# Kernel tuning notes

Hardware: AMD Instinct MI355X
Metric: run time of the kernel (lower is better)

## Reference

```python
import jax, jax.numpy as jnp
import numpy as np
import math

B, S, D, H = 1, 2048, 2048, 16
HD = D // H  # head_dim = 128


def _rotate_half(x):
    h = x.shape[-1] // 2
    return jnp.concatenate([-x[..., h:], x[..., :h]], axis=-1)


def setup_inputs() -> dict:
    key = jax.random.key(0)
    ks = jax.random.split(key, 8)
    hidden_states = jax.random.normal(ks[0], (B, S, D), dtype=jnp.float32)
    # additive causal mask: 0 on/below diagonal, large negative above
    causal = jnp.tril(jnp.ones((S, S), dtype=bool))
    attention_mask = jnp.where(causal, 0.0, -1e9).astype(jnp.float32)[None, None]
    # LLaMA rotary tables for head_dim
    inv_freq = 1.0 / (10000.0 ** (jnp.arange(0, HD, 2, dtype=jnp.float32) / HD))
    t = jnp.arange(S, dtype=jnp.float32)
    freqs = jnp.einsum('s,d->sd', t, inv_freq)          # [S, HD/2]
    emb = jnp.concatenate([freqs, freqs], axis=-1)       # [S, HD]
    cos = jnp.cos(emb)[None, None]                       # [1,1,S,HD]
    sin = jnp.sin(emb)[None, None]
    scale = 1.0 / math.sqrt(D)
    Wq = jax.random.normal(ks[1], (D, D), dtype=jnp.float32) * scale
    Wk = jax.random.normal(ks[2], (D, D), dtype=jnp.float32) * scale
    Wv = jax.random.normal(ks[3], (D, D), dtype=jnp.float32) * scale
    Wo = jax.random.normal(ks[4], (D, D), dtype=jnp.float32) * scale
    # IA3 scales initialized to ones (as in module), perturbed slightly to be non-trivial
    l_k = jnp.ones((1, H, 1, HD), dtype=jnp.float32) + 0.01 * jax.random.normal(ks[5], (1, H, 1, HD), dtype=jnp.float32)
    l_v = jnp.ones((1, H, 1, HD), dtype=jnp.float32) + 0.01 * jax.random.normal(ks[6], (1, H, 1, HD), dtype=jnp.float32)
    return {
        'hidden_states': hidden_states, 'attention_mask': attention_mask,
        'cos': cos, 'sin': sin,
        'Wq': Wq, 'Wk': Wk, 'Wv': Wv, 'Wo': Wo, 'l_k': l_k, 'l_v': l_v,
    }


def reference(hidden_states, attention_mask, cos, sin, Wq, Wk, Wv, Wo, l_k, l_v):
    b, s, d = hidden_states.shape
    h, hd = H, HD
    # projections (nn.Linear: x @ W.T), split heads -> [b, h, s, hd]
    def split_heads(x):
        return x.reshape(b, s, h, hd).transpose(0, 2, 1, 3)
    q = split_heads(hidden_states @ Wq.T)
    k = split_heads(hidden_states @ Wk.T)
    v = split_heads(hidden_states @ Wv.T)
    # RoPE on q and k
    q = q * cos + _rotate_half(q) * sin
    k = k * cos + _rotate_half(k) * sin
    # IA3: note the module scales QUERY by peft_l_k and VALUE by peft_l_v
    q = q * l_k
    v = v * l_v
    # manual attention
    scores = jnp.einsum('bhqd,bhkd->bhqk', q, k) / math.sqrt(hd)
    scores = scores + attention_mask
    attn = jax.nn.softmax(scores.astype(jnp.float32), axis=-1).astype(scores.dtype)
    out = jnp.einsum('bhqk,bhkd->bhqd', attn, v)
    out = out.transpose(0, 2, 1, 3).reshape(b, s, d)
    return out @ Wo.T
```

## Files before the change

kernel.cpp:

```cpp
#include <hip/hip_runtime.h>

typedef __attribute__((ext_vector_type(8))) short short8;
typedef __attribute__((ext_vector_type(4))) short s16x4;
typedef __attribute__((ext_vector_type(4))) float f32x4;
typedef unsigned short ushort;

#define S_LEN 2048
#define D_MODEL 2048
#define NH 16
#define HD 128

__device__ __forceinline__ float b2f(ushort u) {
  union { unsigned int i; float f; } v; v.i = ((unsigned int)u) << 16; return v.f;
}
__device__ __forceinline__ ushort f2b(float f) {
  union { float f; unsigned int i; } v; v.f = f;
  unsigned int r = v.i + 0x7FFFu + ((v.i >> 16) & 1u);
  return (ushort)(r >> 16);
}
__device__ __forceinline__ ushort f2b_trunc(float f) {
  union { float f; unsigned int i; } v; v.f = f;
  return (ushort)(v.i >> 16);
}

__device__ __forceinline__ void gload_lds16(const void* g, void* l) {
  __builtin_amdgcn_global_load_lds(
      (const __attribute__((address_space(1))) void*)g,
      (__attribute__((address_space(3))) void*)l, 16, 0, 0);
}

template<bool C32, bool QKV>
__device__ __forceinline__ void gemm_bf16_body(const ushort* __restrict__ A,
                                               const ushort* __restrict__ B,
                                               void* __restrict__ Cp, int ldc,
                                               const float* __restrict__ lv)
{
  __shared__ ushort lA[128 * 64];
  __shared__ ushort lB[128 * 64];
  const int tid  = threadIdx.x;
  const int lane = tid & 63;
  const int wave = tid >> 6;
  const int quad = lane >> 4;
  const int l15  = lane & 15;
  const int wm   = wave >> 1;
  const int wn   = wave & 1;
  const int m0   = blockIdx.y * 128;
  const int n0   = blockIdx.x * 128;

  f32x4 acc[4][4];
#pragma unroll
  for (int i = 0; i < 4; ++i)
#pragma unroll
    for (int j = 0; j < 4; ++j)
      acc[i][j] = (f32x4){0.f, 0.f, 0.f, 0.f};

  const int srow0 = wave * 8 + (lane >> 3);
  const int cph   = lane & 7;

  for (int kt = 0; kt < 32; ++kt) {
    __syncthreads();
#pragma unroll
    for (int j = 0; j < 4; ++j) {
      const int row = j * 32 + srow0;
      const int gc  = cph ^ (row & 7);
      gload_lds16(A + (size_t)(m0 + row) * 2048 + kt * 64 + gc * 8,
                  &lA[row * 64 + cph * 8]);
      gload_lds16(B + (size_t)(n0 + row) * 2048 + kt * 64 + gc * 8,
                  &lB[row * 64 + cph * 8]);
    }
    __syncthreads();
#pragma unroll
    for (int kk = 0; kk < 2; ++kk) {
      short8 af[4], bfr[4];
#pragma unroll
      for (int i = 0; i < 4; ++i) {
        const int r = wm * 64 + i * 16 + l15;
        af[i] = *(const short8*)&lA[r * 64 + (((kk * 4 + quad) ^ (l15 & 7)) * 8)];
      }
#pragma unroll
      for (int j = 0; j < 4; ++j) {
        const int r = wn * 64 + j * 16 + l15;
        bfr[j] = *(const short8*)&lB[r * 64 + (((kk * 4 + quad) ^ (l15 & 7)) * 8)];
      }
#pragma unroll
      for (int i = 0; i < 4; ++i)
#pragma unroll
        for (int j = 0; j < 4; ++j)
          acc[i][j] = __builtin_amdgcn_mfma_f32_16x16x32_bf16(af[i], bfr[j], acc[i][j], 0, 0, 0);
    }
  }

  if (QKV && n0 >= 4096) {
    ushort* C = (ushort*)Cp;
#pragma unroll
    for (int j = 0; j < 4; ++j)
#pragma unroll
      for (int i = 0; i < 4; ++i) {
        const int vcol = n0 - 4096 + wn * 64 + j * 16 + l15;
        const float sc = lv[vcol];
        const int sb   = m0 + wm * 64 + i * 16 + quad * 4;
        s16x4 pk;
#pragma unroll
        for (int r = 0; r < 4; ++r) pk[r] = (short)f2b(acc[i][j][r] * sc);
        *(s16x4*)&C[(size_t)vcol * 6144 + 4096 + sb] = pk;
      }
    return;
  }

#pragma unroll
  for (int i = 0; i < 4; ++i)
#pragma unroll
    for (int j = 0; j < 4; ++j)
#pragma unroll
      for (int r = 0; r < 4; ++r) {
        const int row = m0 + wm * 64 + i * 16 + quad * 4 + r;
        const int col = n0 + wn * 64 + j * 16 + l15;
        if (C32) ((float*)Cp)[(size_t)row * ldc + col] = acc[i][j][r];
        else     ((ushort*)Cp)[(size_t)row * ldc + col] = f2b(acc[i][j][r]);
      }
}

__global__ __launch_bounds__(256)
void gemm_qkv_b(const ushort* __restrict__ A, const ushort* __restrict__ B,
                ushort* __restrict__ C, const float* __restrict__ lv)
{ gemm_bf16_body<false, true>(A, B, C, 6144, lv); }

__global__ __launch_bounds__(256)
void gemm_bf16_f(const ushort* __restrict__ A, const ushort* __restrict__ B,
                 float* __restrict__ C, int ldc)
{ gemm_bf16_body<true, false>(A, B, C, ldc, nullptr); }

__global__ __launch_bounds__(256)
void cvt_to_bf16(const float* __restrict__ hs, const float* __restrict__ Wq,
                 const float* __restrict__ Wk, const float* __restrict__ Wv,
                 const float* __restrict__ Wo, ushort* __restrict__ dst)
{
  const size_t base = ((size_t)blockIdx.x * 256 + threadIdx.x) * 8;
  const int row = (int)(base >> 11);
  const int col = (int)(base & 2047);
  const float* src;
  if      (row < 2048) src = Wq + (size_t)row * 2048;
  else if (row < 4096) src = Wk + (size_t)(row - 2048) * 2048;
  else if (row < 6144) src = Wv + (size_t)(row - 4096) * 2048;
  else if (row < 8192) src = Wo + (size_t)(row - 6144) * 2048;
  else                 src = hs + (size_t)(row - 8192) * 2048;
  float4 a = *(const float4*)(src + col);
  float4 b = *(const float4*)(src + col + 4);
  short8 s;
  s[0] = (short)f2b(a.x); s[1] = (short)f2b(a.y);
  s[2] = (short)f2b(a.z); s[3] = (short)f2b(a.w);
  s[4] = (short)f2b(b.x); s[5] = (short)f2b(b.y);
  s[6] = (short)f2b(b.z); s[7] = (short)f2b(b.w);
  *(short8*)(dst + base) = s;
}

__global__ __launch_bounds__(256)
void rope_qk(ushort* __restrict__ arena,
             const float* __restrict__ cosb, const float* __restrict__ sinb,
             const float* __restrict__ lk)
{
  const int s = blockIdx.x;
  const float qscale = 0.08838834764831845f * 1.4426950408889634f;
#pragma unroll
  for (int i = 0; i < 4; ++i) {
    const int p = threadIdx.x + 256 * i;
    const int h = p >> 6;
    const int d = p & 63;

    const size_t qlo_i = (size_t)s * 6144 + h * HD + d;
    const size_t klo_i = qlo_i + 2048;
    const float c_lo = cosb[s * HD + d];
    const float c_hi = cosb[s * HD + d + 64];
    const float s_lo = sinb[s * HD + d];
    const float s_hi = sinb[s * HD + d + 64];

    const float qlo = b2f(arena[qlo_i]), qhi = b2f(arena[qlo_i + 64]);
    const float klo = b2f(arena[klo_i]), khi = b2f(arena[klo_i + 64]);

    const float rq_lo = qlo * c_lo - qhi * s_lo;
    const float rq_hi = qhi * c_hi + qlo * s_hi;
    const float rk_lo = klo * c_lo - khi * s_lo;
    const float rk_hi = khi * c_hi + klo * s_hi;

    arena[qlo_i]      = f2b(rq_lo * lk[h * HD + d]      * qscale);
    arena[qlo_i + 64] = f2b(rq_hi * lk[h * HD + d + 64] * qscale);
    arena[klo_i]      = f2b(rk_lo);
    arena[klo_i + 64] = f2b(rk_hi);
  }
}

__device__ const int FA_QT[30]   = {5,11,11,10,10,15,15,4,9,9,13,14,14,14,15,8,8,12,12,13,13,3,7,7,12,6,6,2,1,0};
__device__ const int FA_BEG[30]  = {0,0,12,0,11,10,21,0,0,10,18,0,10,20,0,0,9,8,17,0,9,0,0,8,0,0,7,0,0,0};
__device__ const int FA_END[30]  = {12,12,24,11,22,21,32,10,10,20,28,10,20,30,10,9,18,17,26,9,18,8,8,16,8,7,14,6,4,2};
__device__ const int FA_SLOT[30] = {5,16,17,14,15,28,29,4,12,13,23,24,25,26,27,10,11,19,20,21,22,3,8,9,18,6,7,2,1,0};
__device__ const int FA_OFF[16]  = {0,1,2,3,4,5,6,8,10,12,14,16,18,21,24,27};
__device__ const int FA_NC[16]   = {1,1,1,1,1,1,2,2,2,2,2,2,3,3,3,3};

__global__ __launch_bounds__(256, 2)
void flash_attn2(const ushort* __restrict__ arena,
                 ushort* __restrict__ Opart,
                 float* __restrict__ Ml)
{
  __shared__ ushort Kl[64 * 128];
  __shared__ ushort Vt[128 * 64];
  __shared__ ushort Pl[4][32 * 72];

  const int tid  = threadIdx.x;
  const int lane = tid & 63;
  const int w    = tid >> 6;
  const int quad = lane >> 4;
  const int l15  = lane & 15;
  const int h    = blockIdx.y;

  const int item  = blockIdx.x;
  const int qt    = FA_QT[item];
  const int ktBeg = FA_BEG[item];
  const int ktEnd = FA_END[item];
  const int slot  = h * 30 + FA_SLOT[item];

  short8 qa[2][4];
#pragma unroll
  for (int i = 0; i < 2; ++i)
#pragma unroll
    for (int kk = 0; kk < 4; ++kk)
      qa[i][kk] = *(const short8*)(arena +
          (size_t)(qt * 128 + w * 32 + i * 16 + l15) * 6144 + h * HD + kk * 32 + quad * 8);

  f32x4 o[2][8], acc_l[2];
#pragma unroll
  for (int i = 0; i < 2; ++i) {
    acc_l[i] = (f32x4){0.f, 0.f, 0.f, 0.f};
#pragma unroll
    for (int nf = 0; nf < 8; ++nf) o[i][nf] = (f32x4){0.f, 0.f, 0.f, 0.f};
  }

  short8 bones;
#pragma unroll
  for (int e = 0; e < 8; ++e) bones[e] = (short)0x3F80;

  const int ksrow0 = w * 4 + (lane >> 4);
  const int kch    = lane & 15;
  const int vrow0  = w * 8 + (lane >> 3);
  const int vch    = lane & 7;

  for (int kt = ktBeg; kt < ktEnd; ++kt) {
    __syncthreads();

#pragma unroll
    for (int j = 0; j < 4; ++j) {
      const int row = j * 16 + ksrow0;
      const int gc  = kch ^ (row & 15);
      gload_lds16(arena + (size_t)(kt * 64 + row) * 6144 + 2048 + h * HD + gc * 8,
                  &Kl[row * 128 + kch * 8]);
    }
#pragma unroll
    for (int j = 0; j < 4; ++j) {
      const int d  = j * 32 + vrow0;
      const int gc = vch ^ (d & 7);
      gload_lds16(arena + (size_t)(h * HD + d) * 6144 + 4096 + kt * 64 + gc * 8,
                  &Vt[d * 64 + vch * 8]);
    }
    __syncthreads();

    f32x4 sf[2][4];
#pragma unroll
    for (int i = 0; i < 2; ++i)
#pragma unroll
      for (int n = 0; n < 4; ++n) sf[i][n] = (f32x4){0.f, 0.f, 0.f, 0.f};
#pragma unroll
    for (int kk = 0; kk < 4; ++kk)
#pragma unroll
      for (int n = 0; n < 4; ++n) {
        const int key = n * 16 + l15;
        short8 b = *(const short8*)&Kl[key * 128 + (((kk * 4 + quad) ^ l15) * 8)];
#pragma unroll
        for (int i = 0; i < 2; ++i)
          sf[i][n] = __builtin_amdgcn_mfma_f32_16x16x32_bf16(qa[i][kk], b, sf[i][n], 0, 0, 0);
      }

    if (kt >= 2 * qt) {
#pragma unroll
      for (int i = 0; i < 2; ++i)
#pragma unroll
        for (int n = 0; n < 4; ++n)
#pragma unroll
          for (int r = 0; r < 4; ++r) {
            const int key = kt * 64 + n * 16 + l15;
            const int row = qt * 128 + w * 32 + i * 16 + quad * 4 + r;
            if (key > row) sf[i][n][r] = -1e30f;
          }
    }

#pragma unroll
    for (int i = 0; i < 2; ++i)
#pragma unroll
      for (int n = 0; n < 4; ++n)
#pragma unroll
        for (int r = 0; r < 4; ++r)
          Pl[w][(i * 16 + quad * 4 + r) * 72 + n * 16 + l15] = f2b_trunc(exp2f(sf[i][n][r]));

#pragma unroll
    for (int kk = 0; kk < 2; ++kk) {
      short8 pa[2];
#pragma unroll
      for (int i = 0; i < 2; ++i)
        pa[i] = *(const short8*)&Pl[w][(i * 16 + l15) * 72 + kk * 32 + quad * 8];
#pragma unroll
      for (int nf = 0; nf < 8; ++nf) {
        const int d = nf * 16 + l15;
        short8 b = *(const short8*)&Vt[d * 64 + (((kk * 4 + quad) ^ (l15 & 7)) * 8)];
#pragma unroll
        for (int i = 0; i < 2; ++i)
          o[i][nf] = __builtin_amdgcn_mfma_f32_16x16x32_bf16(pa[i], b, o[i][nf], 0, 0, 0);
      }
#pragma unroll
      for (int i = 0; i < 2; ++i)
        acc_l[i] = __builtin_amdgcn_mfma_f32_16x16x32_bf16(pa[i], bones, acc_l[i], 0, 0, 0);
    }
  }

  ushort* dst = Opart + (size_t)slot * (128 * 128);
#pragma unroll
  for (int i = 0; i < 2; ++i)
#pragma unroll
    for (int nf = 0; nf < 8; ++nf)
#pragma unroll
      for (int r = 0; r < 4; ++r) {
        const int row = w * 32 + i * 16 + quad * 4 + r;
        const int col = nf * 16 + l15;
        dst[row * 128 + col] = f2b(o[i][nf][r]);
      }
  if (l15 == 0) {
#pragma unroll
    for (int i = 0; i < 2; ++i)
#pragma unroll
      for (int r = 0; r < 4; ++r)
        Ml[(size_t)slot * 128 + w * 32 + i * 16 + quad * 4 + r] = acc_l[i][r];
  }
}

__global__ __launch_bounds__(256)
void fa_combine2(const ushort* __restrict__ Opart, const float* __restrict__ Ml,
                 ushort* __restrict__ Ab)
{
  const int qt  = blockIdx.x;
  const int h   = blockIdx.y;
  const int row = threadIdx.x >> 1;
  const int hf  = (threadIdx.x & 1) * 64;
  const int np  = FA_NC[qt];
  const int s0  = h * 30 + FA_OFF[qt];

  float lsum = 0.f;
  for (int c = 0; c < np; ++c) lsum += Ml[(size_t)(s0 + c) * 128 + row];
  const float inv = 1.0f / lsum;

  float acc[64];
#pragma unroll
  for (int e = 0; e < 64; ++e) acc[e] = 0.f;
  for (int c = 0; c < np; ++c) {
    const ushort* src = Opart + (size_t)(s0 + c) * (128 * 128) + row * 128 + hf;
#pragma unroll
    for (int j = 0; j < 8; ++j) {
      short8 x = *(const short8*)(src + j * 8);
#pragma unroll
      for (int e = 0; e < 8; ++e) acc[j * 8 + e] += b2f((ushort)x[e]);
    }
  }
  ushort* d = Ab + (size_t)(qt * 128 + row) * 2048 + h * 128 + hf;
#pragma unroll
  for (int j = 0; j < 8; ++j) {
    short8 y;
#pragma unroll
    for (int e = 0; e < 8; ++e) y[e] = (short)f2b(acc[j * 8 + e] * inv);
    *(short8*)(d + j * 8) = y;
  }
}

template<bool A32, bool B32, bool C32>
__device__ __forceinline__ void gemm_body(const void* __restrict__ Ap,
                                          const void* __restrict__ Bp,
                                          void* __restrict__ Cp)
{
  __shared__ ushort lA[128 * 72];
  __shared__ ushort lB[128 * 72];
  const int tid  = threadIdx.x;
  const int lane = tid & 63;
  const int wave = tid >> 6;
  const int quad = lane >> 4;
  const int l15  = lane & 15;
  const int wm   = wave >> 1;
  const int wn   = wave & 1;
  const int m0   = blockIdx.y * 128;
  const int n0   = blockIdx.x * 128;

  f32x4 acc[4][4];
#pragma unroll
  for (int i = 0; i < 4; ++i)
#pragma unroll
    for (int j = 0; j < 4; ++j)
      acc[i][j] = (f32x4){0.f, 0.f, 0.f, 0.f};

  const int srow = tid >> 1;
  const int scol = (tid & 1) * 32;
  ushort* aL = &lA[srow * 72 + scol];
  ushort* bL = &lB[srow * 72 + scol];

  for (int kt = 0; kt < 32; ++kt) {
    __syncthreads();
    if (A32) {
      const float* g = (const float*)Ap + (size_t)(m0 + srow) * 2048 + kt * 64 + scol;
#pragma unroll
      for (int j = 0; j < 4; ++j) {
        float4 f0 = *(const float4*)(g + 8 * j);
        float4 f1 = *(const float4*)(g + 8 * j + 4);
        short8 sv;
        sv[0] = (short)f2b(f0.x); sv[1] = (short)f2b(f0.y);
        sv[2] = (short)f2b(f0.z); sv[3] = (short)f2b(f0.w);
        sv[4] = (short)f2b(f1.x); sv[5] = (short)f2b(f1.y);
        sv[6] = (short)f2b(f1.z); sv[7] = (short)f2b(f1.w);
        *(short8*)(aL + 8 * j) = sv;
      }
    } else {
      const ushort* g = (const ushort*)Ap + (size_t)(m0 + srow) * 2048 + kt * 64 + scol;
#pragma unroll
      for (int j = 0; j < 4; ++j)
        *(short8*)(aL + 8 * j) = *(const short8*)(g + 8 * j);
    }
    if (B32) {
      const float* g = (const float*)Bp + (size_t)(n0 + srow) * 2048 + kt * 64 + scol;
#pragma unroll
      for (int j = 0; j < 4; ++j) {
        float4 f0 = *(const float4*)(g + 8 * j);
        float4 f1 = *(const float4*)(g + 8 * j + 4);
        short8 sv;
        sv[0] = (short)f2b(f0.x); sv[1] = (short)f2b(f0.y);
        sv[2] = (short)f2b(f0.z); sv[3] = (short)f2b(f0.w);
        sv[4] = (short)f2b(f1.x); sv[5] = (short)f2b(f1.y);
        sv[6] = (short)f2b(f1.z); sv[7] = (short)f2b(f1.w);
        *(short8*)(bL + 8 * j) = sv;
      }
    } else {
      const ushort* g = (const ushort*)Bp + (size_t)(n0 + srow) * 2048 + kt * 64 + scol;
#pragma unroll
      for (int j = 0; j < 4; ++j)
        *(short8*)(bL + 8 * j) = *(const short8*)(g + 8 * j);
    }
    __syncthreads();
#pragma unroll
    for (int kk = 0; kk < 2; ++kk) {
      short8 af[4], bfr[4];
#pragma unroll
      for (int i = 0; i < 4; ++i)
        af[i] = *(const short8*)&lA[(wm * 64 + i * 16 + l15) * 72 + kk * 32 + quad * 8];
#pragma unroll
      for (int j = 0; j < 4; ++j)
        bfr[j] = *(const short8*)&lB[(wn * 64 + j * 16 + l15) * 72 + kk * 32 + quad * 8];
#pragma unroll
      for (int i = 0; i < 4; ++i)
#pragma unroll
        for (int j = 0; j < 4; ++j)
          acc[i][j] = __builtin_amdgcn_mfma_f32_16x16x32_bf16(af[i], bfr[j], acc[i][j], 0, 0, 0);
    }
  }

#pragma unroll
  for (int i = 0; i < 4; ++i)
#pragma unroll
    for (int j = 0; j < 4; ++j)
#pragma unroll
      for (int r = 0; r < 4; ++r) {
        const int row = m0 + wm * 64 + i * 16 + quad * 4 + r;
        const int col = n0 + wn * 64 + j * 16 + l15;
        if (C32) ((float*)Cp)[(size_t)row * 2048 + col] = acc[i][j][r];
        else     ((ushort*)Cp)[(size_t)row * 2048 + col] = f2b(acc[i][j][r]);
      }
}

__global__ __launch_bounds__(256)
void gemm_qkv_f32(const float* __restrict__ A, const float* __restrict__ Bq,
                  const float* __restrict__ Bk, const float* __restrict__ Bv,
                  ushort* __restrict__ Cq, ushort* __restrict__ Ck, ushort* __restrict__ Cv)
{
  const float* B = (blockIdx.z == 0) ? Bq : (blockIdx.z == 1 ? Bk : Bv);
  ushort* C      = (blockIdx.z == 0) ? Cq : (blockIdx.z == 1 ? Ck : Cv);
  gemm_body<true, true, false>(A, B, C);
}

__global__ __launch_bounds__(256)
void gemm_wo_f32(const ushort* __restrict__ A, const float* __restrict__ B,
                 float* __restrict__ C)
{ gemm_body<false, true, true>(A, B, C); }

__global__ __launch_bounds__(256)
void rope_ia3_old(ushort* __restrict__ base, int stride, int koff, int voff,
                  const float* __restrict__ cosb, const float* __restrict__ sinb,
                  const float* __restrict__ lk, const float* __restrict__ lv)
{
  const int s = blockIdx.x;
  const float qscale = 0.08838834764831845f * 1.4426950408889634f;
#pragma unroll
  for (int i = 0; i < 4; ++i) {
    const int p = threadIdx.x + 256 * i;
    const int h = p >> 6;
    const int d = p & 63;
    const size_t lo = (size_t)s * stride + h * HD + d;
    const size_t hi = lo + 64;
    const float c_lo = cosb[s * HD + d];
    const float c_hi = cosb[s * HD + d + 64];
    const float s_lo = sinb[s * HD + d];
    const float s_hi = sinb[s * HD + d + 64];
    ushort* Q = base;
    ushort* K = base + koff;
    ushort* V = base + voff;
    const float qlo = b2f(Q[lo]), qhi = b2f(Q[hi]);
    const float klo = b2f(K[lo]), khi = b2f(K[hi]);
    const float vlo = b2f(V[lo]), vhi = b2f(V[hi]);
    const float rq_lo = qlo * c_lo - qhi * s_lo;
    const float rq_hi = qhi * c_hi + qlo * s_hi;
    const float rk_lo = klo * c_lo - khi * s_lo;
    const float rk_hi = khi * c_hi + klo * s_hi;
    Q[lo] = f2b(rq_lo * lk[h * HD + d]      * qscale);
    Q[hi] = f2b(rq_hi * lk[h * HD + d + 64] * qscale);
    K[lo] = f2b(rk_lo);
    K[hi] = f2b(rk_hi);
    V[lo] = f2b(vlo * lv[h * HD + d]);
    V[hi] = f2b(vhi * lv[h * HD + d + 64]);
  }
}

__global__ __launch_bounds__(256)
void flash_attn_old(const ushort* __restrict__ QKV, int stride, int koff, int voff,
                    ushort* __restrict__ Ob, int ostride)
{
  __shared__ ushort Kl[64 * 128];
  __shared__ ushort Vt[128 * 64];
  __shared__ ushort Pl[4][16 * 72];

  const int tid  = threadIdx.x;
  const int lane = tid & 63;
  const int w    = tid >> 6;
  const int quad = lane >> 4;
  const int l15  = lane & 15;
  const int qt   = (int)gridDim.x - 1 - (int)blockIdx.x;
  const int h    = blockIdx.y;

  const ushort* Q = QKV;
  const ushort* K = QKV + koff;
  const ushort* V = QKV + voff;

  const int qrow = qt * 64 + w * 16 + l15;
  short8 qa[4];
#pragma unroll
  for (int kk = 0; kk < 4; ++kk)
    qa[kk] = *(const short8*)(Q + (size_t)qrow * stride + h * HD + kk * 32 + quad * 8);

  float m_[4], l_[4];
  f32x4 o[8];
#pragma unroll
  for (int r = 0; r < 4; ++r) { m_[r] = -1e30f; l_[r] = 0.f; }
#pragma unroll
  for (int nf = 0; nf < 8; ++nf) o[nf] = (f32x4){0.f, 0.f, 0.f, 0.f};

  const int ksrow0 = w * 4 + (lane >> 4);
  const int kch    = lane & 15;
  const int vkp    = tid & 15;
  const int vd8    = tid >> 4;

  for (int kt = 0; kt <= qt; ++kt) {
    __syncthreads();
#pragma unroll
    for (int j = 0; j < 4; ++j) {
      const int row = j * 16 + ksrow0;
      const int gc  = kch ^ (row & 15);
      gload_lds16(K + (size_t)(kt * 64 + row) * stride + h * HD + gc * 8,
                  &Kl[row * 128 + kch * 8]);
    }
    {
      const ushort* vb = V + (size_t)(kt * 64) * stride + h * HD + vd8 * 8;
      short8 v0 = *(const short8*)(vb + (size_t)(2 * vkp)      * stride);
      short8 v1 = *(const short8*)(vb + (size_t)(2 * vkp + 1)  * stride);
      short8 v2 = *(const short8*)(vb + (size_t)(2 * vkp + 32) * stride);
      short8 v3 = *(const short8*)(vb + (size_t)(2 * vkp + 33) * stride);
      const int wlo = vkp >> 2, woff = 2 * (vkp & 3);
#pragma unroll
      for (int c = 0; c < 8; ++c) {
        const int d = vd8 * 8 + c;
        unsigned int p01 = (ushort)v0[c] | ((unsigned int)(ushort)v1[c] << 16);
        unsigned int p23 = (ushort)v2[c] | ((unsigned int)(ushort)v3[c] << 16);
        *(unsigned int*)&Vt[d * 64 + ((wlo       ^ c) * 8) + woff] = p01;
        *(unsigned int*)&Vt[d * 64 + (((wlo + 4) ^ c) * 8) + woff] = p23;
      }
    }
    __syncthreads();

    f32x4 sf[4];
#pragma unroll
    for (int n = 0; n < 4; ++n) sf[n] = (f32x4){0.f, 0.f, 0.f, 0.f};
#pragma unroll
    for (int kk = 0; kk < 4; ++kk)
#pragma unroll
      for (int n = 0; n < 4; ++n) {
        const int key = n * 16 + l15;
        short8 b = *(const short8*)&Kl[key * 128 + (((kk * 4 + quad) ^ l15) * 8)];
        sf[n] = __builtin_amdgcn_mfma_f32_16x16x32_bf16(qa[kk], b, sf[n], 0, 0, 0);
      }

    if (kt == qt) {
#pragma unroll
      for (int n = 0; n < 4; ++n)
#pragma unroll
        for (int r = 0; r < 4; ++r)
          if (n * 16 + l15 > w * 16 + quad * 4 + r) sf[n][r] = -1e30f;
    }

    float pm[4];
#pragma unroll
    for (int r = 0; r < 4; ++r)
      pm[r] = fmaxf(fmaxf(sf[0][r], sf[1][r]), fmaxf(sf[2][r], sf[3][r]));
#pragma unroll
    for (int off = 1; off < 16; off <<= 1)
#pragma unroll
      for (int r = 0; r < 4; ++r)
        pm[r] = fmaxf(pm[r], __shfl_xor(pm[r], off));

    float al[4], ps[4], p[4][4];
#pragma unroll
    for (int r = 0; r < 4; ++r) {
      const float mn = fmaxf(m_[r], pm[r]);
      al[r] = exp2f(m_[r] - mn);
      m_[r] = mn;
      ps[r] = 0.f;
    }
#pragma unroll
    for (int n = 0; n < 4; ++n)
#pragma unroll
      for (int r = 0; r < 4; ++r) {
        p[n][r] = exp2f(sf[n][r] - m_[r]);
        ps[r] += p[n][r];
      }
#pragma unroll
    for (int off = 1; off < 16; off <<= 1)
#pragma unroll
      for (int r = 0; r < 4; ++r)
        ps[r] += __shfl_xor(ps[r], off);
#pragma unroll
    for (int r = 0; r < 4; ++r) l_[r] = al[r] * l_[r] + ps[r];
#pragma unroll
    for (int nf = 0; nf < 8; ++nf)
#pragma unroll
      for (int r = 0; r < 4; ++r) o[nf][r] *= al[r];

#pragma unroll
    for (int n = 0; n < 4; ++n)
#pragma unroll
      for (int r = 0; r < 4; ++r)
        Pl[w][(quad * 4 + r) * 72 + n * 16 + l15] = f2b(p[n][r]);

#pragma unroll
    for (int kk = 0; kk < 2; ++kk) {
      short8 pa = *(const short8*)&Pl[w][l15 * 72 + kk * 32 + quad * 8];
#pragma unroll
      for (int nf = 0; nf < 8; ++nf) {
        const int d = nf * 16 + l15;
        short8 b = *(const short8*)&Vt[d * 64 + (((kk * 4 + quad) ^ (l15 & 7)) * 8)];
        o[nf] = __builtin_amdgcn_mfma_f32_16x16x32_bf16(pa, b, o[nf], 0, 0, 0);
      }
    }
  }

  float inv[4];
#pragma unroll
  for (int r = 0; r < 4; ++r) inv[r] = 1.0f / l_[r];
#pragma unroll
  for (int nf = 0; nf < 8; ++nf)
#pragma unroll
    for (int r = 0; r < 4; ++r) {
      const int row = qt * 64 + w * 16 + quad * 4 + r;
      const int col = h * HD + nf * 16 + l15;
      Ob[(size_t)row * ostride + col] = f2b(o[nf][r] * inv[r]);
    }
}

extern "C" void kernel_launch(void* const* d_in, const int* in_sizes, int n_in,
                              void* d_out, int out_size, void* d_ws, size_t ws_size,
                              hipStream_t stream)
{
  const float* hs   = (const float*)d_in[0];
  const float* cosb = (const float*)d_in[2];
  const float* sinb = (const float*)d_in[3];
  const float* Wq   = (const float*)d_in[4];
  const float* Wk   = (const float*)d_in[5];
  const float* Wv   = (const float*)d_in[6];
  const float* Wo   = (const float*)d_in[7];
  const float* lk   = (const float*)d_in[8];
  const float* lv   = (const float*)d_in[9];
  float* out = (float*)d_out;

  char* ws = (char*)d_ws;
  const bool fast = ws_size >= (size_t)64 * 1024 * 1024;

  if (fast) {
    ushort* WB    = (ushort*)ws;
    ushort* hsB   = WB + (size_t)8192 * 2048;
    ushort* QKV   = (ushort*)(ws + (size_t)40 * 1024 * 1024);
    ushort* Ab    = hsB;
    ushort* Opart = WB;
    float*  Ml    = (float*)(ws + (size_t)16 * 1024 * 1024);

    cvt_to_bf16<<<dim3(10240), 256, 0, stream>>>(hs, Wq, Wk, Wv, Wo, WB);
    gemm_qkv_b<<<dim3(48, 16), 256, 0, stream>>>(hsB, WB, QKV, lv);
    rope_qk<<<dim3(S_LEN), 256, 0, stream>>>(QKV, cosb, sinb, lk);
    flash_attn2<<<dim3(30, NH), 256, 0, stream>>>(QKV, Opart, Ml);
    fa_combine2<<<dim3(16, NH), 256, 0, stream>>>(Opart, Ml, Ab);
    gemm_bf16_f<<<dim3(16, 16), 256, 0, stream>>>(Ab, WB + (size_t)6144 * 2048, out, 2048);
  } else {
    const size_t SZ = (size_t)S_LEN * D_MODEL;
    ushort* Qb = (ushort*)ws;
    ushort* Kb = Qb + SZ;
    ushort* Vb = Qb + 2 * SZ;
    ushort* Ab = Qb;

    gemm_qkv_f32<<<dim3(16, 16, 3), 256, 0, stream>>>(hs, Wq, Wk, Wv, Qb, Kb, Vb);
    rope_ia3_old<<<dim3(S_LEN), 256, 0, stream>>>(Qb, 2048, (int)SZ, (int)(2 * SZ), cosb, sinb, lk, lv);
    flash_attn_old<<<dim3(S_LEN / 64, NH), 256, 0, stream>>>(Qb, 2048, (int)SZ, (int)(2 * SZ), Ab, 2048);
    gemm_wo_f32<<<dim3(16, 16), 256, 0, stream>>>(Ab, Wo, out);
  }
}
```

Before: 311.9 us.

## Fuse RoPE/IA3 into QKV GEMM epilogue and finalize single-chunk attention tiles directly

Q/K column tiles of the QKV GEMM now remap B-fragment columns so each wave holds both the lo and hi halves of the rotary pair, which lets RoPE, the IA3 query scale and the softmax scale be applied in the GEMM epilogue. This removes the separate rope_qk kernel and its read-modify-write pass over Q and K. Attention work items whose query tile has only one chunk now normalize and write straight to the output buffer, and the combine kernel is launched only for tiles 6-15. The epilogue does scalar 2-byte stores and per-element cos/sin loads, which could be slower than the old coalesced path, and Opart aliasing with WB must not collide with the new direct Ab writes.

New measurement: 307.5 us. No clear change (-1.4%).

```diff
diff --git a/kernel.cpp b/kernel.cpp
--- a/kernel.cpp
+++ b/kernel.cpp
@@ -29,11 +29,14 @@
       (__attribute__((address_space(3))) void*)l, 16, 0, 0);
 }
 
-template<bool C32, bool QKV>
+template<bool C32, bool QKVM>
 __device__ __forceinline__ void gemm_bf16_body(const ushort* __restrict__ A,
                                                const ushort* __restrict__ B,
                                                void* __restrict__ Cp, int ldc,
-                                               const float* __restrict__ lv)
+                                               const float* __restrict__ lv,
+                                               const float* __restrict__ cosb,
+                                               const float* __restrict__ sinb,
+                                               const float* __restrict__ lk)
 {
   __shared__ ushort lA[128 * 64];
   __shared__ ushort lB[128 * 64];
@@ -47,6 +50,13 @@
   const int m0   = blockIdx.y * 128;
   const int n0   = blockIdx.x * 128;
 
+  const bool isV = QKVM && (n0 >= 4096);
+  int bcol[4];
+#pragma unroll
+  for (int j = 0; j < 4; ++j)
+    bcol[j] = (QKVM && !isV) ? (wn * 32 + (j & 1) * 16 + (j >> 1) * 64)
+                             : (wn * 64 + j * 16);
+
   f32x4 acc[4][4];
 #pragma unroll
   for (int i = 0; i < 4; ++i)
@@ -79,7 +89,7 @@
       }
 #pragma unroll
       for (int j = 0; j < 4; ++j) {
-        const int r = wn * 64 + j * 16 + l15;
+        const int r = bcol[j] + l15;
         bfr[j] = *(const short8*)&lB[r * 64 + (((kk * 4 + quad) ^ (l15 & 7)) * 8)];
       }
 #pragma unroll
@@ -90,20 +100,48 @@
     }
   }
 
-  if (QKV && n0 >= 4096) {
+  if (QKVM) {
     ushort* C = (ushort*)Cp;
-#pragma unroll
-    for (int j = 0; j < 4; ++j)
-#pragma unroll
-      for (int i = 0; i < 4; ++i) {
-        const int vcol = n0 - 4096 + wn * 64 + j * 16 + l15;
-        const float sc = lv[vcol];
-        const int sb   = m0 + wm * 64 + i * 16 + quad * 4;
-        s16x4 pk;
-#pragma unroll
-        for (int r = 0; r < 4; ++r) pk[r] = (short)f2b(acc[i][j][r] * sc);
-        *(s16x4*)&C[(size_t)vcol * 6144 + 4096 + sb] = pk;
-      }
+    if (isV) {
+#pragma unroll
+      for (int j = 0; j < 4; ++j)
+#pragma unroll
+        for (int i = 0; i < 4; ++i) {
+          const int vcol = n0 - 4096 + bcol[j] + l15;
+          const float sc = lv[vcol];
+          const int sb   = m0 + wm * 64 + i * 16 + quad * 4;
+          s16x4 pk;
+#pragma unroll
+          for (int r = 0; r < 4; ++r) pk[r] = (short)f2b(acc[i][j][r] * sc);
+          *(s16x4*)&C[(size_t)vcol * 6144 + 4096 + sb] = pk;
+        }
+    } else {
+      const bool isQ = (n0 < 2048);
+      const int hb = n0 & 2047;
+      const float qsc = 0.08838834764831845f * 1.4426950408889634f;
+#pragma unroll
+      for (int i = 0; i < 4; ++i)
+#pragma unroll
+        for (int j = 0; j < 2; ++j) {
+          const int d_lo = bcol[j] + l15;
+          const int d_hi = d_lo + 64;
+          const float sl_lo = isQ ? lk[hb + d_lo] * qsc : 1.f;
+          const float sl_hi = isQ ? lk[hb + d_hi] * qsc : 1.f;
+#pragma unroll
+          for (int r = 0; r < 4; ++r) {
+            const int s = m0 + wm * 64 + i * 16 + quad * 4 + r;
+            const float c_lo = cosb[s * HD + d_lo], s_lo = sinb[s * HD + d_lo];
+            const float c_hi = cosb[s * HD + d_hi], s_hi = sinb[s * HD + d_hi];
+            const float lo = acc[i][j][r];
+            const float hi = acc[i][j + 2][r];
+            float o_lo = lo * c_lo - hi * s_lo;
+            float o_hi = hi * c_hi + lo * s_hi;
+            if (isQ) { o_lo *= sl_lo; o_hi *= sl_hi; }
+            C[(size_t)s * 6144 + n0 + d_lo] = f2b(o_lo);
+            C[(size_t)s * 6144 + n0 + d_hi] = f2b(o_hi);
+          }
+        }
+    }
     return;
   }
 
@@ -114,7 +152,7 @@
 #pragma unroll
       for (int r = 0; r < 4; ++r) {
         const int row = m0 + wm * 64 + i * 16 + quad * 4 + r;
-        const int col = n0 + wn * 64 + j * 16 + l15;
+        const int col = n0 + bcol[j] + l15;
         if (C32) ((float*)Cp)[(size_t)row * ldc + col] = acc[i][j][r];
         else     ((ushort*)Cp)[(size_t)row * ldc + col] = f2b(acc[i][j][r]);
       }
@@ -122,13 +160,15 @@
 
 __global__ __launch_bounds__(256)
 void gemm_qkv_b(const ushort* __restrict__ A, const ushort* __restrict__ B,
-                ushort* __restrict__ C, const float* __restrict__ lv)
-{ gemm_bf16_body<false, true>(A, B, C, 6144, lv); }
+                ushort* __restrict__ C, const float* __restrict__ lv,
+                const float* __restrict__ cosb, const float* __restrict__ sinb,
+                const float* __restrict__ lk)
+{ gemm_bf16_body<false, true>(A, B, C, 6144, lv, cosb, sinb, lk); }
 
 __global__ __launch_bounds__(256)
 void gemm_bf16_f(const ushort* __restrict__ A, const ushort* __restrict__ B,
                  float* __restrict__ C, int ldc)
-{ gemm_bf16_body<true, false>(A, B, C, ldc, nullptr); }
+{ gemm_bf16_body<true, false>(A, B, C, ldc, nullptr, nullptr, nullptr, nullptr); }
 
 __global__ __launch_bounds__(256)
 void cvt_to_bf16(const float* __restrict__ hs, const float* __restrict__ Wq,
@@ -154,41 +194,6 @@
   *(short8*)(dst + base) = s;
 }
 
-__global__ __launch_bounds__(256)
-void rope_qk(ushort* __restrict__ arena,
-             const float* __restrict__ cosb, const float* __restrict__ sinb,
-             const float* __restrict__ lk)
-{
-  const int s = blockIdx.x;
-  const float qscale = 0.08838834764831845f * 1.4426950408889634f;
-#pragma unroll
-  for (int i = 0; i < 4; ++i) {
-    const int p = threadIdx.x + 256 * i;
-    const int h = p >> 6;
-    const int d = p & 63;
-
-    const size_t qlo_i = (size_t)s * 6144 + h * HD + d;
-    const size_t klo_i = qlo_i + 2048;
-    const float c_lo = cosb[s * HD + d];
-    const float c_hi = cosb[s * HD + d + 64];
-    const float s_lo = sinb[s * HD + d];
-    const float s_hi = sinb[s * HD + d + 64];
-
-    const float qlo = b2f(arena[qlo_i]), qhi = b2f(arena[qlo_i + 64]);
-    const float klo = b2f(arena[klo_i]), khi = b2f(arena[klo_i + 64]);
-
-    const float rq_lo = qlo * c_lo - qhi * s_lo;
-    const float rq_hi = qhi * c_hi + qlo * s_hi;
-    const float rk_lo = klo * c_lo - khi * s_lo;
-    const float rk_hi = khi * c_hi + klo * s_hi;
-
-    arena[qlo_i]      = f2b(rq_lo * lk[h * HD + d]      * qscale);
-    arena[qlo_i + 64] = f2b(rq_hi * lk[h * HD + d + 64] * qscale);
-    arena[klo_i]      = f2b(rk_lo);
-    arena[klo_i + 64] = f2b(rk_hi);
-  }
-}
-
 __device__ const int FA_QT[30]   = {5,11,11,10,10,15,15,4,9,9,13,14,14,14,15,8,8,12,12,13,13,3,7,7,12,6,6,2,1,0};
 __device__ const int FA_BEG[30]  = {0,0,12,0,11,10,21,0,0,10,18,0,10,20,0,0,9,8,17,0,9,0,0,8,0,0,7,0,0,0};
 __device__ const int FA_END[30]  = {12,12,24,11,22,21,32,10,10,20,28,10,20,30,10,9,18,17,26,9,18,8,8,16,8,7,14,6,4,2};
@@ -198,6 +203,7 @@
 
 __global__ __launch_bounds__(256, 2)
 void flash_attn2(const ushort* __restrict__ arena,
+                 ushort* __restrict__ Ab,
                  ushort* __restrict__ Opart,
                  float* __restrict__ Ml)
 {
@@ -319,23 +325,41 @@
     }
   }
 
-  ushort* dst = Opart + (size_t)slot * (128 * 128);
-#pragma unroll
-  for (int i = 0; i < 2; ++i)
-#pragma unroll
-    for (int nf = 0; nf < 8; ++nf)
-#pragma unroll
-      for (int r = 0; r < 4; ++r) {
-        const int row = w * 32 + i * 16 + quad * 4 + r;
-        const int col = nf * 16 + l15;
-        dst[row * 128 + col] = f2b(o[i][nf][r]);
-      }
-  if (l15 == 0) {
+  if (FA_NC[qt] == 1) {
+    float inv[2][4];
 #pragma unroll
     for (int i = 0; i < 2; ++i)
 #pragma unroll
-      for (int r = 0; r < 4; ++r)
-        Ml[(size_t)slot * 128 + w * 32 + i * 16 + quad * 4 + r] = acc_l[i][r];
+      for (int r = 0; r < 4; ++r) inv[i][r] = 1.0f / acc_l[i][r];
+#pragma unroll
+    for (int i = 0; i < 2; ++i)
+#pragma unroll
+      for (int nf = 0; nf < 8; ++nf)
+#pragma unroll
+        for (int r = 0; r < 4; ++r) {
+          const int row = qt * 128 + w * 32 + i * 16 + quad * 4 + r;
+          const int col = h * HD + nf * 16 + l15;
+          Ab[(size_t)row * 2048 + col] = f2b(o[i][nf][r] * inv[i][r]);
+        }
+  } else {
+    ushort* dst = Opart + (size_t)slot * (128 * 128);
+#pragma unroll
+    for (int i = 0; i < 2; ++i)
+#pragma unroll
+      for (int nf = 0; nf < 8; ++nf)
+#pragma unroll
+        for (int r = 0; r < 4; ++r) {
+          const int row = w * 32 + i * 16 + quad * 4 + r;
+          const int col = nf * 16 + l15;
+          dst[row * 128 + col] = f2b(o[i][nf][r]);
+        }
+    if (l15 == 0) {
+#pragma unroll
+      for (int i = 0; i < 2; ++i)
+#pragma unroll
+        for (int r = 0; r < 4; ++r)
+          Ml[(size_t)slot * 128 + w * 32 + i * 16 + quad * 4 + r] = acc_l[i][r];
+    }
   }
 }
 
@@ -343,7 +367,7 @@
 void fa_combine2(const ushort* __restrict__ Opart, const float* __restrict__ Ml,
                  ushort* __restrict__ Ab)
 {
-  const int qt  = blockIdx.x;
+  const int qt  = 6 + blockIdx.x;
   const int h   = blockIdx.y;
   const int row = threadIdx.x >> 1;
   const int hf  = (threadIdx.x & 1) * 64;
@@ -708,10 +732,9 @@
     float*  Ml    = (float*)(ws + (size_t)16 * 1024 * 1024);
 
     cvt_to_bf16<<<dim3(10240), 256, 0, stream>>>(hs, Wq, Wk, Wv, Wo, WB);
-    gemm_qkv_b<<<dim3(48, 16), 256, 0, stream>>>(hsB, WB, QKV, lv);
-    rope_qk<<<dim3(S_LEN), 256, 0, stream>>>(QKV, cosb, sinb, lk);
-    flash_attn2<<<dim3(30, NH), 256, 0, stream>>>(QKV, Opart, Ml);
-    fa_combine2<<<dim3(16, NH), 256, 0, stream>>>(Opart, Ml, Ab);
+    gemm_qkv_b<<<dim3(48, 16), 256, 0, stream>>>(hsB, WB, QKV, lv, cosb, sinb, lk);
+    flash_attn2<<<dim3(30, NH), 256, 0, stream>>>(QKV, Ab, Opart, Ml);
+    fa_combine2<<<dim3(10, NH), 256, 0, stream>>>(Opart, Ml, Ab);
     gemm_bf16_f<<<dim3(16, 16), 256, 0, stream>>>(Ab, WB + (size_t)6144 * 2048, out, 2048);
   } else {
     const size_t SZ = (size_t)S_LEN * D_MODEL;
```

## Split-K the output projection with atomics and write single-chunk attention tiles directly

Applied to the files above, without the earlier changes.

The Wo GEMM is split into two K halves launched as a 3D grid that accumulate into the float output with atomic adds. This raises the grid from 256 to 512 blocks for better CU occupancy, and the output is zeroed by extra blocks appended to the conversion kernel. Flash attention tiles whose query tile needs only one chunk now normalize and write directly into the attention buffer, so the combine kernel handles only the remaining 10 query tiles. The cost is atomic traffic, extra zeroing writes, and a summation order that is no longer deterministic.

After: 314.7 us. No clear change (+0.9%).

```diff
diff --git a/kernel.cpp b/kernel.cpp
--- a/kernel.cpp
+++ b/kernel.cpp
@@ -29,11 +29,12 @@
       (__attribute__((address_space(3))) void*)l, 16, 0, 0);
 }
 
-template<bool C32, bool QKV>
+template<bool C32, bool QKVM, bool ATOM>
 __device__ __forceinline__ void gemm_bf16_body(const ushort* __restrict__ A,
                                                const ushort* __restrict__ B,
                                                void* __restrict__ Cp, int ldc,
-                                               const float* __restrict__ lv)
+                                               const float* __restrict__ lv,
+                                               int ktBeg, int ktEnd)
 {
   __shared__ ushort lA[128 * 64];
   __shared__ ushort lB[128 * 64];
@@ -57,7 +58,7 @@
   const int srow0 = wave * 8 + (lane >> 3);
   const int cph   = lane & 7;
 
-  for (int kt = 0; kt < 32; ++kt) {
+  for (int kt = ktBeg; kt < ktEnd; ++kt) {
     __syncthreads();
 #pragma unroll
     for (int j = 0; j < 4; ++j) {
@@ -90,7 +91,7 @@
     }
   }
 
-  if (QKV && n0 >= 4096) {
+  if (QKVM && n0 >= 4096) {
     ushort* C = (ushort*)Cp;
 #pragma unroll
     for (int j = 0; j < 4; ++j)
@@ -115,26 +116,37 @@
       for (int r = 0; r < 4; ++r) {
         const int row = m0 + wm * 64 + i * 16 + quad * 4 + r;
         const int col = n0 + wn * 64 + j * 16 + l15;
-        if (C32) ((float*)Cp)[(size_t)row * ldc + col] = acc[i][j][r];
-        else     ((ushort*)Cp)[(size_t)row * ldc + col] = f2b(acc[i][j][r]);
+        if (ATOM)     unsafeAtomicAdd(&((float*)Cp)[(size_t)row * ldc + col], acc[i][j][r]);
+        else if (C32) ((float*)Cp)[(size_t)row * ldc + col] = acc[i][j][r];
+        else          ((ushort*)Cp)[(size_t)row * ldc + col] = f2b(acc[i][j][r]);
       }
 }
 
 __global__ __launch_bounds__(256)
 void gemm_qkv_b(const ushort* __restrict__ A, const ushort* __restrict__ B,
                 ushort* __restrict__ C, const float* __restrict__ lv)
-{ gemm_bf16_body<false, true>(A, B, C, 6144, lv); }
-
-__global__ __launch_bounds__(256)
-void gemm_bf16_f(const ushort* __restrict__ A, const ushort* __restrict__ B,
-                 float* __restrict__ C, int ldc)
-{ gemm_bf16_body<true, false>(A, B, C, ldc, nullptr); }
+{ gemm_bf16_body<false, true, false>(A, B, C, 6144, lv, 0, 32); }
+
+__global__ __launch_bounds__(256)
+void gemm_wo_sk(const ushort* __restrict__ A, const ushort* __restrict__ B,
+                float* __restrict__ C)
+{
+  const int z = blockIdx.z;
+  gemm_bf16_body<true, false, true>(A, B, C, 2048, nullptr, z * 16, z * 16 + 16);
+}
 
 __global__ __launch_bounds__(256)
 void cvt_to_bf16(const float* __restrict__ hs, const float* __restrict__ Wq,
                  const float* __restrict__ Wk, const float* __restrict__ Wv,
-                 const float* __restrict__ Wo, ushort* __restrict__ dst)
-{
+                 const float* __restrict__ Wo, ushort* __restrict__ dst,
+                 float* __restrict__ outz)
+{
+  if (blockIdx.x >= 10240) {
+    const size_t base = ((size_t)(blockIdx.x - 10240) * 256 + threadIdx.x) * 8;
+    *(float4*)(outz + base)     = (float4){0.f, 0.f, 0.f, 0.f};
+    *(float4*)(outz + base + 4) = (float4){0.f, 0.f, 0.f, 0.f};
+    return;
+  }
   const size_t base = ((size_t)blockIdx.x * 256 + threadIdx.x) * 8;
   const int row = (int)(base >> 11);
   const int col = (int)(base & 2047);
@@ -198,6 +210,7 @@
 
 __global__ __launch_bounds__(256, 2)
 void flash_attn2(const ushort* __restrict__ arena,
+                 ushort* __restrict__ Ab,
                  ushort* __restrict__ Opart,
                  float* __restrict__ Ml)
 {
@@ -319,23 +332,41 @@
     }
   }
 
-  ushort* dst = Opart + (size_t)slot * (128 * 128);
-#pragma unroll
-  for (int i = 0; i < 2; ++i)
-#pragma unroll
-    for (int nf = 0; nf < 8; ++nf)
-#pragma unroll
-      for (int r = 0; r < 4; ++r) {
-        const int row = w * 32 + i * 16 + quad * 4 + r;
-        const int col = nf * 16 + l15;
-        dst[row * 128 + col] = f2b(o[i][nf][r]);
-      }
-  if (l15 == 0) {
+  if (FA_NC[qt] == 1) {
+    float inv[2][4];
 #pragma unroll
     for (int i = 0; i < 2; ++i)
 #pragma unroll
-      for (int r = 0; r < 4; ++r)
-        Ml[(size_t)slot * 128 + w * 32 + i * 16 + quad * 4 + r] = acc_l[i][r];
+      for (int r = 0; r < 4; ++r) inv[i][r] = 1.0f / acc_l[i][r];
+#pragma unroll
+    for (int i = 0; i < 2; ++i)
+#pragma unroll
+      for (int nf = 0; nf < 8; ++nf)
+#pragma unroll
+        for (int r = 0; r < 4; ++r) {
+          const int row = qt * 128 + w * 32 + i * 16 + quad * 4 + r;
+          const int col = h * HD + nf * 16 + l15;
+          Ab[(size_t)row * 2048 + col] = f2b(o[i][nf][r] * inv[i][r]);
+        }
+  } else {
+    ushort* dst = Opart + (size_t)slot * (128 * 128);
+#pragma unroll
+    for (int i = 0; i < 2; ++i)
+#pragma unroll
+      for (int nf = 0; nf < 8; ++nf)
+#pragma unroll
+        for (int r = 0; r < 4; ++r) {
+          const int row = w * 32 + i * 16 + quad * 4 + r;
+          const int col = nf * 16 + l15;
+          dst[row * 128 + col] = f2b(o[i][nf][r]);
+        }
+    if (l15 == 0) {
+#pragma unroll
+      for (int i = 0; i < 2; ++i)
+#pragma unroll
+        for (int r = 0; r < 4; ++r)
+          Ml[(size_t)slot * 128 + w * 32 + i * 16 + quad * 4 + r] = acc_l[i][r];
+    }
   }
 }
 
@@ -343,7 +374,7 @@
 void fa_combine2(const ushort* __restrict__ Opart, const float* __restrict__ Ml,
                  ushort* __restrict__ Ab)
 {
-  const int qt  = blockIdx.x;
+  const int qt  = 6 + blockIdx.x;
   const int h   = blockIdx.y;
   const int row = threadIdx.x >> 1;
   const int hf  = (threadIdx.x & 1) * 64;
@@ -707,12 +738,12 @@
     ushort* Opart = WB;
     float*  Ml    = (float*)(ws + (size_t)16 * 1024 * 1024);
 
-    cvt_to_bf16<<<dim3(10240), 256, 0, stream>>>(hs, Wq, Wk, Wv, Wo, WB);
+    cvt_to_bf16<<<dim3(12288), 256, 0, stream>>>(hs, Wq, Wk, Wv, Wo, WB, out);
     gemm_qkv_b<<<dim3(48, 16), 256, 0, stream>>>(hsB, WB, QKV, lv);
     rope_qk<<<dim3(S_LEN), 256, 0, stream>>>(QKV, cosb, sinb, lk);
-    flash_attn2<<<dim3(30, NH), 256, 0, stream>>>(QKV, Opart, Ml);
-    fa_combine2<<<dim3(16, NH), 256, 0, stream>>>(Opart, Ml, Ab);
-    gemm_bf16_f<<<dim3(16, 16), 256, 0, stream>>>(Ab, WB + (size_t)6144 * 2048, out, 2048);
+    flash_attn2<<<dim3(30, NH), 256, 0, stream>>>(QKV, Ab, Opart, Ml);
+    fa_combine2<<<dim3(10, NH), 256, 0, stream>>>(Opart, Ml, Ab);
+    gemm_wo_sk<<<dim3(16, 16, 2), 256, 0, stream>>>(Ab, WB + (size_t)6144 * 2048, out);
   } else {
     const size_t SZ = (size_t)S_LEN * D_MODEL;
     ushort* Qb = (ushort*)ws;
```
